# Kernel tuning notes

Hardware: AMD Instinct MI355X
Metric: run time of the kernel (lower is better)

## Reference

```python
import jax, jax.numpy as jnp
import numpy as np

N = 50000      # nodes
E = 800000     # edges (avg degree 16)
D = 128        # node_dim
H = 128        # hidden_dim
ED = 16        # edge_dim (unused by GCNConv, kept for signature fidelity)
G = 64         # graphs in batch
EPS = 1e-5     # BatchNorm eps


def setup_inputs() -> dict:
    key = jax.random.key(0)
    ks = jax.random.split(key, 16)
    s = 0.05
    inp = {
        "x": jax.random.normal(ks[0], (N, D), jnp.float32),
        "edge_index": jax.random.randint(ks[1], (2, E), 0, N, dtype=jnp.int64),
        "edge_attr": jax.random.normal(ks[2], (E, ED), jnp.float32),
        "batch": jnp.sort(jax.random.randint(ks[3], (N,), 0, G, dtype=jnp.int64)),
        # GCNConv weights/biases
        "W1": jax.random.normal(ks[4], (D, H), jnp.float32) * s,
        "b1": jnp.zeros((H,), jnp.float32),
        "W2": jax.random.normal(ks[5], (H, H), jnp.float32) * s,
        "b2": jnp.zeros((H,), jnp.float32),
        "W3": jax.random.normal(ks[6], (H, H), jnp.float32) * s,
        "b3": jnp.zeros((H,), jnp.float32),
        # BatchNorm affine params (training-mode batch stats)
        "g1": jnp.ones((H,), jnp.float32), "be1": jnp.zeros((H,), jnp.float32),
        "g2": jnp.ones((H,), jnp.float32), "be2": jnp.zeros((H,), jnp.float32),
        "g3": jnp.ones((H,), jnp.float32), "be3": jnp.zeros((H,), jnp.float32),
    }
    return inp


def reference(x, edge_index, edge_attr, batch,
              W1, b1, W2, b2, W3, b3,
              g1, be1, g2, be2, g3, be3):
    n = x.shape[0]
    src, dst = edge_index[0], edge_index[1]

    # GCN symmetric normalization with added self-loops:
    # deg[i] = 1 + in_degree(i); norm(e) = deg[src]^-1/2 * deg[dst]^-1/2
    deg = jax.ops.segment_sum(jnp.ones((src.shape[0],), x.dtype), dst,
                              num_segments=n) + 1.0
    dinv = jax.lax.rsqrt(deg)
    edge_norm = (dinv[src] * dinv[dst])[:, None]   # [E,1]
    self_norm = (dinv * dinv)[:, None]             # [N,1] self-loop weight

    def gcn(h, W, b):
        h = h @ W                                  # [N,H]
        agg = jax.ops.segment_sum(h[src] * edge_norm, dst, num_segments=n)
        return agg + h * self_norm + b

    def bn_sigmoid(h, g, b):
        m = h.mean(0)
        v = jnp.mean(jnp.square(h - m), 0)         # biased variance (torch BN)
        return jax.nn.sigmoid((h - m) * jax.lax.rsqrt(v + EPS) * g + b)

    h = bn_sigmoid(gcn(x, W1, b1), g1, be1)
    h = bn_sigmoid(gcn(h, W2, b2), g2, be2)
    h = bn_sigmoid(gcn(h, W3, b3), g3, be3)

    # global_mean_pool over graph ids
    cnt = jax.ops.segment_sum(jnp.ones((n,), h.dtype), batch, num_segments=G)
    pooled = jax.ops.segment_sum(h, batch, num_segments=G)
    return pooled / jnp.maximum(cnt, 1.0)[:, None]
```

## Files before the change

kernel.cpp:

```cpp
#include <hip/hip_runtime.h>
#include <math.h>

#define NDIM 128

typedef __attribute__((ext_vector_type(8))) short short8;
typedef __attribute__((ext_vector_type(4))) float f32x4;

__device__ __forceinline__ float sigmoidf_(float x){ return 1.0f/(1.0f + __expf(-x)); }

__device__ __forceinline__ unsigned short f2bf(float f){
  unsigned u = __float_as_uint(f);
  unsigned r = (u + 0x7fffu + ((u >> 16) & 1u)) >> 16;
  return (unsigned short)r;
}

__global__ void deg_count_k(const int* __restrict__ dst, int* __restrict__ counts, int E){
  int e = blockIdx.x*blockDim.x + threadIdx.x;
  if(e < E) atomicAdd(&counts[dst[e]], 1);
}

__global__ void dinv_k(const int* __restrict__ counts, float* __restrict__ dinv, int N){
  int i = blockIdx.x*blockDim.x + threadIdx.x;
  if(i < N) dinv[i] = rsqrtf(1.0f + (float)counts[i]);
}

__global__ void scan1_k(const int* __restrict__ counts, int* __restrict__ scanned,
                        int* __restrict__ chunksums, int N){
  __shared__ int lds[256];
  int t = threadIdx.x; int idx = blockIdx.x*256 + t;
  int x = (idx < N) ? counts[idx] : 0;
  lds[t] = x; __syncthreads();
  for(int o=1;o<256;o<<=1){
    int v = (t>=o) ? lds[t-o] : 0;
    __syncthreads();
    lds[t] += v;
    __syncthreads();
  }
  if(idx < N) scanned[idx] = lds[t];
  if(t == 255) chunksums[blockIdx.x] = lds[255];
}

__global__ void scan2_k(int* __restrict__ chunksums, int nchunks){
  __shared__ int lds[256];
  int t = threadIdx.x;
  int x = (t < nchunks) ? chunksums[t] : 0;
  lds[t] = x; __syncthreads();
  for(int o=1;o<256;o<<=1){
    int v = (t>=o) ? lds[t-o] : 0;
    __syncthreads();
    lds[t] += v;
    __syncthreads();
  }
  if(t < nchunks) chunksums[t] = lds[t] - x;
}

__global__ void scan3_k(const int* __restrict__ scanned, const int* __restrict__ counts,
                        const int* __restrict__ chunksums, int* __restrict__ row_start, int N){
  int i = blockIdx.x*blockDim.x + threadIdx.x;
  if(i < N) row_start[i] = scanned[i] - counts[i] + chunksums[i>>8];
}

__global__ void fill_k(const int* __restrict__ src, const int* __restrict__ dst,
                       const float* __restrict__ dinv, const int* __restrict__ row_start,
                       int* __restrict__ cursor, int* __restrict__ csr_src,
                       float* __restrict__ csr_norm, int E){
  int e = blockIdx.x*blockDim.x + threadIdx.x;
  if(e >= E) return;
  int d = dst[e], s = src[e];
  int pos = row_start[d] + atomicAdd(&cursor[d], 1);
  csr_src[pos] = s;
  csr_norm[pos] = dinv[s]*dinv[d];
}

__global__ void bounds_k(const int* __restrict__ batch, int* __restrict__ bound, int N, int G){
  int g = threadIdx.x;
  if(g > G) return;
  int lo = 0, hi = N;
  while(lo < hi){ int mid = (lo+hi)>>1; if(batch[mid] < g) lo = mid+1; else hi = mid; }
  bound[g] = lo;
}

__global__ void wprep_k(const float* __restrict__ W0, const float* __restrict__ W1,
                        const float* __restrict__ W2, unsigned short* __restrict__ Wsw){
  int t = blockIdx.x*256 + threadIdx.x;
  if(t >= 3*16384) return;
  int l = t >> 14; int i = t & 16383;
  const float* W = (l==0) ? W0 : ((l==1) ? W1 : W2);
  int k = i >> 7, n = i & 127;
  Wsw[l*16384 + (((k>>3)*128 + n)<<3) + (k&7)] = f2bf(W[k*128+n]);
}

__global__ __launch_bounds__(256) void gemm_mfma_k(const float* __restrict__ A,
                                                   const unsigned short* __restrict__ Wsw,
                                                   unsigned short* __restrict__ Bh,
                                                   const float* __restrict__ scale,
                                                   const float* __restrict__ shift,
                                                   int N){
  __shared__ unsigned short Al[16384];
  __shared__ unsigned short Wl[16384];
  int t = threadIdx.x;
  int row0 = blockIdx.x * 128;
  bool bn = (scale != nullptr);

  #pragma unroll
  for(int i=0;i<8;i++){
    int u = t + i*256;
    *(uint4*)&Wl[u<<3] = *(const uint4*)&Wsw[u<<3];
  }
  int o = t & 15, rbase = t >> 4;
  #pragma unroll
  for(int it=0; it<8; it++){
    int r = rbase + it*16;
    int grow = row0 + r;
    float4 v0 = make_float4(0.f,0.f,0.f,0.f), v1 = v0;
    if(grow < N){
      v0 = *(const float4*)&A[grow*NDIM + o*8];
      v1 = *(const float4*)&A[grow*NDIM + o*8 + 4];
      if(bn){
        float4 sc0 = *(const float4*)&scale[o*8],   sh0 = *(const float4*)&shift[o*8];
        float4 sc1 = *(const float4*)&scale[o*8+4], sh1 = *(const float4*)&shift[o*8+4];
        v0.x = sigmoidf_(v0.x*sc0.x + sh0.x); v0.y = sigmoidf_(v0.y*sc0.y + sh0.y);
        v0.z = sigmoidf_(v0.z*sc0.z + sh0.z); v0.w = sigmoidf_(v0.w*sc0.w + sh0.w);
        v1.x = sigmoidf_(v1.x*sc1.x + sh1.x); v1.y = sigmoidf_(v1.y*sc1.y + sh1.y);
        v1.z = sigmoidf_(v1.z*sc1.z + sh1.z); v1.w = sigmoidf_(v1.w*sc1.w + sh1.w);
      }
    }
    uint4 pk;
    pk.x = (unsigned)f2bf(v0.x) | ((unsigned)f2bf(v0.y)<<16);
    pk.y = (unsigned)f2bf(v0.z) | ((unsigned)f2bf(v0.w)<<16);
    pk.z = (unsigned)f2bf(v1.x) | ((unsigned)f2bf(v1.y)<<16);
    pk.w = (unsigned)f2bf(v1.z) | ((unsigned)f2bf(v1.w)<<16);
    *(uint4*)&Al[(o*128 + r)<<3] = pk;
  }
  __syncthreads();

  int wv = t >> 6, lane = t & 63, quad = lane >> 4, l16 = lane & 15;
  int rw = (wv & 1) * 64, cw = (wv >> 1) * 64;
  f32x4 acc[4][4];
  #pragma unroll
  for(int rt=0;rt<4;rt++)
    #pragma unroll
    for(int ct=0;ct<4;ct++) acc[rt][ct] = (f32x4){0.f,0.f,0.f,0.f};

  #pragma unroll
  for(int ks=0; ks<4; ks++){
    short8 a[4], b[4];
    #pragma unroll
    for(int rt=0;rt<4;rt++)
      a[rt] = *(short8*)&Al[(((ks*4+quad)*128) + rw + rt*16 + l16) << 3];
    #pragma unroll
    for(int ct=0;ct<4;ct++)
      b[ct] = *(short8*)&Wl[(((ks*4+quad)*128) + cw + ct*16 + l16) << 3];
    #pragma unroll
    for(int rt=0;rt<4;rt++)
      #pragma unroll
      for(int ct=0;ct<4;ct++)
        acc[rt][ct] = __builtin_amdgcn_mfma_f32_16x16x32_bf16(a[rt], b[ct], acc[rt][ct], 0, 0, 0);
  }

  #pragma unroll
  for(int rt=0;rt<4;rt++){
    int gr = row0 + rw + rt*16 + quad*4;
    #pragma unroll
    for(int ct=0;ct<4;ct++){
      int col = cw + ct*16 + l16;
      #pragma unroll
      for(int reg=0;reg<4;reg++){
        if(gr + reg < N) Bh[(gr+reg)*NDIM + col] = f2bf(acc[rt][ct][reg]);
      }
    }
  }
}

__global__ void agg_k(const unsigned int* __restrict__ hb,
                      const float* __restrict__ dinv,
                      const int* __restrict__ row_start, const int* __restrict__ counts,
                      const int* __restrict__ csr_src, const float* __restrict__ csr_norm,
                      const float* __restrict__ bias, float* __restrict__ hC, int N){
  int i = blockIdx.x;
  if(i >= N) return;
  int t = threadIdx.x;
  int rs = row_start[i], cnt = counts[i];
  float2 acc = make_float2(0.f, 0.f);
  int j = rs;
  for(; j+1 < rs+cnt; j += 2){
    int s0 = csr_src[j],   s1 = csr_src[j+1];
    float n0 = csr_norm[j], n1 = csr_norm[j+1];
    unsigned u0 = hb[s0*64 + t];
    unsigned u1 = hb[s1*64 + t];
    acc.x += n0*__uint_as_float(u0<<16) + n1*__uint_as_float(u1<<16);
    acc.y += n0*__uint_as_float(u0 & 0xffff0000u) + n1*__uint_as_float(u1 & 0xffff0000u);
  }
  if(j < rs+cnt){
    int s = csr_src[j]; float nm = csr_norm[j];
    unsigned u = hb[s*64 + t];
    acc.x += nm*__uint_as_float(u<<16);
    acc.y += nm*__uint_as_float(u & 0xffff0000u);
  }
  float di = dinv[i]; float sn = di*di;
  unsigned su = hb[i*64 + t];
  float2 bv = *(const float2*)&bias[t*2];
  float2 o;
  o.x = acc.x + sn*__uint_as_float(su<<16)           + bv.x;
  o.y = acc.y + sn*__uint_as_float(su & 0xffff0000u) + bv.y;
  *(float2*)&hC[i*NDIM + t*2] = o;
}

__global__ void stats_k(const float* __restrict__ h, float* __restrict__ sums,
                        float* __restrict__ sumsq, int N){
  __shared__ float ls[256], lq[256];
  int t = threadIdx.x;
  int f = t & 127, half = t >> 7;
  int rowsPerBlock = (N + gridDim.x - 1)/gridDim.x;
  int r0 = blockIdx.x * rowsPerBlock;
  int r1 = min(N, r0 + rowsPerBlock);
  float s=0.f, q=0.f;
  for(int r=r0+half; r<r1; r+=2){
    float v = h[r*NDIM + f];
    s += v; q += v*v;
  }
  ls[t]=s; lq[t]=q; __syncthreads();
  if(t < 128){
    s = ls[t] + ls[t+128];
    q = lq[t] + lq[t+128];
    atomicAdd(&sums[f], s);
    atomicAdd(&sumsq[f], q);
  }
}

__global__ void finalize_k(const float* __restrict__ sums, const float* __restrict__ sumsq,
                           const float* __restrict__ g, const float* __restrict__ be,
                           float* __restrict__ scale, float* __restrict__ shift, int N){
  int f = threadIdx.x;
  float invN = 1.0f/(float)N;
  float m = sums[f]*invN;
  float var = fmaxf(sumsq[f]*invN - m*m, 0.f);
  float s = g[f]*rsqrtf(var + 1e-5f);
  scale[f] = s;
  shift[f] = be[f] - m*s;
}

#define PCH 128
__global__ __launch_bounds__(256) void pool_k(const float* __restrict__ hC,
                                              const int* __restrict__ batch,
                                              const float* __restrict__ scale,
                                              const float* __restrict__ shift,
                                              float* __restrict__ out, int N){
  int t = threadIdx.x;
  int f = t & 127, half = t >> 7;
  int r0 = blockIdx.x*PCH + half;
  int r1 = min(N, blockIdx.x*PCH + PCH);
  float sc = scale[f], sh = shift[f];
  float acc = 0.f; int cur = -1;
  for(int r = r0; r < r1; r += 2){
    int g = batch[r];
    if(g != cur){
      if(cur >= 0) atomicAdd(&out[cur*NDIM + f], acc);
      acc = 0.f; cur = g;
    }
    acc += sigmoidf_(hC[r*NDIM + f]*sc + sh);
  }
  if(cur >= 0) atomicAdd(&out[cur*NDIM + f], acc);
}

__global__ void div_k(float* __restrict__ out, const int* __restrict__ bound){
  int g = blockIdx.x, f = threadIdx.x;
  float cnt = (float)(bound[g+1] - bound[g]);
  out[g*NDIM + f] /= fmaxf(cnt, 1.0f);
}

extern "C" void kernel_launch(void* const* d_in, const int* in_sizes, int n_in,
                              void* d_out, int out_size, void* d_ws, size_t ws_size,
                              hipStream_t stream){
  const float* x     = (const float*)d_in[0];
  const int*   ei    = (const int*)d_in[1];
  const int*   batch = (const int*)d_in[3];
  const float* W [3] = {(const float*)d_in[4], (const float*)d_in[6], (const float*)d_in[8]};
  const float* bi[3] = {(const float*)d_in[5], (const float*)d_in[7], (const float*)d_in[9]};
  const float* gg[3] = {(const float*)d_in[10], (const float*)d_in[12], (const float*)d_in[14]};
  const float* bb[3] = {(const float*)d_in[11], (const float*)d_in[13], (const float*)d_in[15]};

  int N = in_sizes[0] / NDIM;
  int E = in_sizes[1] / 2;
  int G = out_size / NDIM;
  const int* src = ei;
  const int* dst = ei + E;

  char* p = (char*)d_ws;
  auto alloc = [&](size_t bytes)->void*{
    void* r = (void*)p; p += (bytes + 255) & ~(size_t)255; return r;
  };
  unsigned short* hB  = (unsigned short*)alloc((size_t)N*NDIM*2);
  unsigned short* Wsw = (unsigned short*)alloc(3*16384*2);
  float* hC        = (float*)alloc((size_t)N*NDIM*4);
  int*   counts    = (int*)  alloc((size_t)N*4);
  int*   cursor    = (int*)  alloc((size_t)N*4);
  int*   scanned   = (int*)  alloc((size_t)N*4);
  int*   chunksums = (int*)  alloc(256*4);
  int*   row_start = (int*)  alloc((size_t)N*4);
  float* dinv      = (float*)alloc((size_t)N*4);
  int*   csr_src   = (int*)  alloc((size_t)E*4);
  float* csr_norm  = (float*)alloc((size_t)E*4);
  float* sums      = (float*)alloc(3*128*4);
  float* sumsq     = (float*)alloc(3*128*4);
  float* scale     = (float*)alloc(3*128*4);
  float* shift     = (float*)alloc(3*128*4);
  int*   bound     = (int*)  alloc(256*4);

  hipMemsetAsync(counts, 0, (size_t)N*4, stream);
  hipMemsetAsync(cursor, 0, (size_t)N*4, stream);
  hipMemsetAsync(sums,  0, 3*128*4, stream);
  hipMemsetAsync(sumsq, 0, 3*128*4, stream);
  hipMemsetAsync(d_out, 0, (size_t)out_size*4, stream);

  deg_count_k<<<(E+255)/256, 256, 0, stream>>>(dst, counts, E);
  dinv_k<<<(N+255)/256, 256, 0, stream>>>(counts, dinv, N);

  int nchunks = (N+255)/256;
  scan1_k<<<nchunks, 256, 0, stream>>>(counts, scanned, chunksums, N);
  scan2_k<<<1, 256, 0, stream>>>(chunksums, nchunks);
  scan3_k<<<(N+255)/256, 256, 0, stream>>>(scanned, counts, chunksums, row_start, N);
  fill_k<<<(E+255)/256, 256, 0, stream>>>(src, dst, dinv, row_start, cursor, csr_src, csr_norm, E);
  bounds_k<<<1, 128, 0, stream>>>(batch, bound, N, G);
  wprep_k<<<(3*16384+255)/256, 256, 0, stream>>>(W[0], W[1], W[2], Wsw);

  const float* hin = x;
  for(int l=0; l<3; l++){
    const float* sc = (l == 0) ? nullptr : (scale + (l-1)*128);
    const float* sh = (l == 0) ? nullptr : (shift + (l-1)*128);
    gemm_mfma_k<<<(N+127)/128, 256, 0, stream>>>(hin, Wsw + l*16384, hB, sc, sh, N);
    agg_k<<<N, 64, 0, stream>>>((const unsigned int*)hB, dinv, row_start, counts,
                                csr_src, csr_norm, bi[l], hC, N);
    stats_k<<<400, 256, 0, stream>>>(hC, sums + l*128, sumsq + l*128, N);
    finalize_k<<<1, 128, 0, stream>>>(sums + l*128, sumsq + l*128, gg[l], bb[l],
                                      scale + l*128, shift + l*128, N);
    hin = hC;
  }

  pool_k<<<(N+PCH-1)/PCH, 256, 0, stream>>>(hC, batch, scale + 2*128, shift + 2*128,
                                            (float*)d_out, N);
  div_k<<<G, 128, 0, stream>>>((float*)d_out, bound);
}
```

Before: 499.3 us.

## Pack CSR src/norm into uint2 and split wave across two edges per step

The CSR source index and edge norm are stored interleaved as one 8-byte record, so each edge needs one load instead of two separate arrays. The aggregation kernel now has each half-wave handle a different edge, each lane reading 8 bytes (4 bf16 features) per gather, with the loop unrolled 4 deep. The two halves are combined with a cross-lane shuffle at the end. This is meant to raise memory-level parallelism and cut the count of gather instructions, in exchange for a shuffle reduction and half the lanes sitting idle during the final write.

```diff
diff --git a/kernel.cpp b/kernel.cpp
--- a/kernel.cpp
+++ b/kernel.cpp
@@ -62,14 +62,15 @@
 
 __global__ void fill_k(const int* __restrict__ src, const int* __restrict__ dst,
                        const float* __restrict__ dinv, const int* __restrict__ row_start,
-                       int* __restrict__ cursor, int* __restrict__ csr_src,
-                       float* __restrict__ csr_norm, int E){
+                       int* __restrict__ cursor, uint2* __restrict__ csr, int E){
   int e = blockIdx.x*blockDim.x + threadIdx.x;
   if(e >= E) return;
   int d = dst[e], s = src[e];
   int pos = row_start[d] + atomicAdd(&cursor[d], 1);
-  csr_src[pos] = s;
-  csr_norm[pos] = dinv[s]*dinv[d];
+  uint2 rec;
+  rec.x = (unsigned)s;
+  rec.y = __float_as_uint(dinv[s]*dinv[d]);
+  csr[pos] = rec;
 }
 
 __global__ void bounds_k(const int* __restrict__ batch, int* __restrict__ bound, int N, int G){
@@ -172,38 +173,48 @@
   }
 }
 
-__global__ void agg_k(const unsigned int* __restrict__ hb,
+__global__ void agg_k(const uint2* __restrict__ hb2,
                       const float* __restrict__ dinv,
                       const int* __restrict__ row_start, const int* __restrict__ counts,
-                      const int* __restrict__ csr_src, const float* __restrict__ csr_norm,
+                      const uint2* __restrict__ csr,
                       const float* __restrict__ bias, float* __restrict__ hC, int N){
   int i = blockIdx.x;
   if(i >= N) return;
-  int t = threadIdx.x;
+  int lane = threadIdx.x;
+  int h = lane & 31, half = lane >> 5;
   int rs = row_start[i], cnt = counts[i];
-  float2 acc = make_float2(0.f, 0.f);
-  int j = rs;
-  for(; j+1 < rs+cnt; j += 2){
-    int s0 = csr_src[j],   s1 = csr_src[j+1];
-    float n0 = csr_norm[j], n1 = csr_norm[j+1];
-    unsigned u0 = hb[s0*64 + t];
-    unsigned u1 = hb[s1*64 + t];
-    acc.x += n0*__uint_as_float(u0<<16) + n1*__uint_as_float(u1<<16);
-    acc.y += n0*__uint_as_float(u0 & 0xffff0000u) + n1*__uint_as_float(u1 & 0xffff0000u);
-  }
-  if(j < rs+cnt){
-    int s = csr_src[j]; float nm = csr_norm[j];
-    unsigned u = hb[s*64 + t];
-    acc.x += nm*__uint_as_float(u<<16);
-    acc.y += nm*__uint_as_float(u & 0xffff0000u);
-  }
-  float di = dinv[i]; float sn = di*di;
-  unsigned su = hb[i*64 + t];
-  float2 bv = *(const float2*)&bias[t*2];
-  float2 o;
-  o.x = acc.x + sn*__uint_as_float(su<<16)           + bv.x;
-  o.y = acc.y + sn*__uint_as_float(su & 0xffff0000u) + bv.y;
-  *(float2*)&hC[i*NDIM + t*2] = o;
+  int re = rs + cnt;
+  float a0=0.f, a1=0.f, a2=0.f, a3=0.f;
+  for(int j0 = rs; j0 < re; j0 += 8){
+    #pragma unroll
+    for(int q=0; q<4; q++){
+      int j = j0 + 2*q + half;
+      if(j < re){
+        uint2 rec = csr[j];
+        float nm = __uint_as_float(rec.y);
+        uint2 u = hb2[(size_t)rec.x*32 + h];
+        a0 += nm*__uint_as_float(u.x<<16);
+        a1 += nm*__uint_as_float(u.x & 0xffff0000u);
+        a2 += nm*__uint_as_float(u.y<<16);
+        a3 += nm*__uint_as_float(u.y & 0xffff0000u);
+      }
+    }
+  }
+  a0 += __shfl(a0, h + 32);
+  a1 += __shfl(a1, h + 32);
+  a2 += __shfl(a2, h + 32);
+  a3 += __shfl(a3, h + 32);
+  if(half == 0){
+    float di = dinv[i], sn = di*di;
+    uint2 su = hb2[(size_t)i*32 + h];
+    float4 bv = *(const float4*)&bias[h*4];
+    float4 o;
+    o.x = a0 + sn*__uint_as_float(su.x<<16)           + bv.x;
+    o.y = a1 + sn*__uint_as_float(su.x & 0xffff0000u) + bv.y;
+    o.z = a2 + sn*__uint_as_float(su.y<<16)           + bv.z;
+    o.w = a3 + sn*__uint_as_float(su.y & 0xffff0000u) + bv.w;
+    *(float4*)&hC[i*NDIM + h*4] = o;
+  }
 }
 
 __global__ void stats_k(const float* __restrict__ h, float* __restrict__ sums,
@@ -299,8 +310,7 @@
   int*   chunksums = (int*)  alloc(256*4);
   int*   row_start = (int*)  alloc((size_t)N*4);
   float* dinv      = (float*)alloc((size_t)N*4);
-  int*   csr_src   = (int*)  alloc((size_t)E*4);
-  float* csr_norm  = (float*)alloc((size_t)E*4);
+  uint2* csr       = (uint2*)alloc((size_t)E*8);
   float* sums      = (float*)alloc(3*128*4);
   float* sumsq     = (float*)alloc(3*128*4);
   float* scale     = (float*)alloc(3*128*4);
@@ -320,7 +330,7 @@
   scan1_k<<<nchunks, 256, 0, stream>>>(counts, scanned, chunksums, N);
   scan2_k<<<1, 256, 0, stream>>>(chunksums, nchunks);
   scan3_k<<<(N+255)/256, 256, 0, stream>>>(scanned, counts, chunksums, row_start, N);
-  fill_k<<<(E+255)/256, 256, 0, stream>>>(src, dst, dinv, row_start, cursor, csr_src, csr_norm, E);
+  fill_k<<<(E+255)/256, 256, 0, stream>>>(src, dst, dinv, row_start, cursor, csr, E);
   bounds_k<<<1, 128, 0, stream>>>(batch, bound, N, G);
   wprep_k<<<(3*16384+255)/256, 256, 0, stream>>>(W[0], W[1], W[2], Wsw);
 
@@ -329,8 +339,8 @@
     const float* sc = (l == 0) ? nullptr : (scale + (l-1)*128);
     const float* sh = (l == 0) ? nullptr : (shift + (l-1)*128);
     gemm_mfma_k<<<(N+127)/128, 256, 0, stream>>>(hin, Wsw + l*16384, hB, sc, sh, N);
-    agg_k<<<N, 64, 0, stream>>>((const unsigned int*)hB, dinv, row_start, counts,
-                                csr_src, csr_norm, bi[l], hC, N);
+    agg_k<<<N, 64, 0, stream>>>((const uint2*)hB, dinv, row_start, counts,
+                                csr, bi[l], hC, N);
     stats_k<<<400, 256, 0, stream>>>(hC, sums + l*128, sumsq + l*128, N);
     finalize_k<<<1, 128, 0, stream>>>(sums + l*128, sumsq + l*128, gg[l], bb[l],
                                       scale + l*128, shift + l*128, N);
```

Result: slower. 538.5 us (+7.9%).

## Fuse BatchNorm stats into aggregation, pack CSR records, 4 rows per block

Applied to the files above, without the earlier changes.

Packs CSR source index and edge norm into one 8-byte record so each edge needs a single load. The aggregation kernel now processes four nodes per 256-thread block with a 4-way unrolled edge loop. It also accumulates per-feature sum and sum-of-squares in LDS and flushes them with global atomics, which removes the separate stats kernel and its full re-read of hC. The cost is LDS atomic contention and more global atomics (one flush per block, about 12.5k blocks) compared with the old 400-block stats pass.

```diff
diff --git a/kernel.cpp b/kernel.cpp
--- a/kernel.cpp
+++ b/kernel.cpp
@@ -62,14 +62,15 @@
 
 __global__ void fill_k(const int* __restrict__ src, const int* __restrict__ dst,
                        const float* __restrict__ dinv, const int* __restrict__ row_start,
-                       int* __restrict__ cursor, int* __restrict__ csr_src,
-                       float* __restrict__ csr_norm, int E){
+                       int* __restrict__ cursor, uint2* __restrict__ csr, int E){
   int e = blockIdx.x*blockDim.x + threadIdx.x;
   if(e >= E) return;
   int d = dst[e], s = src[e];
   int pos = row_start[d] + atomicAdd(&cursor[d], 1);
-  csr_src[pos] = s;
-  csr_norm[pos] = dinv[s]*dinv[d];
+  uint2 rec;
+  rec.x = (unsigned)s;
+  rec.y = __float_as_uint(dinv[s]*dinv[d]);
+  csr[pos] = rec;
 }
 
 __global__ void bounds_k(const int* __restrict__ batch, int* __restrict__ bound, int N, int G){
@@ -172,59 +173,59 @@
   }
 }
 
-__global__ void agg_k(const unsigned int* __restrict__ hb,
+__global__ __launch_bounds__(256) void agg_k(const unsigned int* __restrict__ hb,
                       const float* __restrict__ dinv,
                       const int* __restrict__ row_start, const int* __restrict__ counts,
-                      const int* __restrict__ csr_src, const float* __restrict__ csr_norm,
-                      const float* __restrict__ bias, float* __restrict__ hC, int N){
-  int i = blockIdx.x;
-  if(i >= N) return;
+                      const uint2* __restrict__ csr,
+                      const float* __restrict__ bias, float* __restrict__ hC,
+                      float* __restrict__ sums, float* __restrict__ sumsq, int N){
+  __shared__ float ls[NDIM], lq[NDIM];
   int t = threadIdx.x;
-  int rs = row_start[i], cnt = counts[i];
-  float2 acc = make_float2(0.f, 0.f);
-  int j = rs;
-  for(; j+1 < rs+cnt; j += 2){
-    int s0 = csr_src[j],   s1 = csr_src[j+1];
-    float n0 = csr_norm[j], n1 = csr_norm[j+1];
-    unsigned u0 = hb[s0*64 + t];
-    unsigned u1 = hb[s1*64 + t];
-    acc.x += n0*__uint_as_float(u0<<16) + n1*__uint_as_float(u1<<16);
-    acc.y += n0*__uint_as_float(u0 & 0xffff0000u) + n1*__uint_as_float(u1 & 0xffff0000u);
-  }
-  if(j < rs+cnt){
-    int s = csr_src[j]; float nm = csr_norm[j];
-    unsigned u = hb[s*64 + t];
-    acc.x += nm*__uint_as_float(u<<16);
-    acc.y += nm*__uint_as_float(u & 0xffff0000u);
-  }
-  float di = dinv[i]; float sn = di*di;
-  unsigned su = hb[i*64 + t];
-  float2 bv = *(const float2*)&bias[t*2];
-  float2 o;
-  o.x = acc.x + sn*__uint_as_float(su<<16)           + bv.x;
-  o.y = acc.y + sn*__uint_as_float(su & 0xffff0000u) + bv.y;
-  *(float2*)&hC[i*NDIM + t*2] = o;
-}
-
-__global__ void stats_k(const float* __restrict__ h, float* __restrict__ sums,
-                        float* __restrict__ sumsq, int N){
-  __shared__ float ls[256], lq[256];
-  int t = threadIdx.x;
-  int f = t & 127, half = t >> 7;
-  int rowsPerBlock = (N + gridDim.x - 1)/gridDim.x;
-  int r0 = blockIdx.x * rowsPerBlock;
-  int r1 = min(N, r0 + rowsPerBlock);
-  float s=0.f, q=0.f;
-  for(int r=r0+half; r<r1; r+=2){
-    float v = h[r*NDIM + f];
-    s += v; q += v*v;
-  }
-  ls[t]=s; lq[t]=q; __syncthreads();
-  if(t < 128){
-    s = ls[t] + ls[t+128];
-    q = lq[t] + lq[t+128];
-    atomicAdd(&sums[f], s);
-    atomicAdd(&sumsq[f], q);
+  if(t < NDIM){ ls[t] = 0.f; lq[t] = 0.f; }
+  __syncthreads();
+
+  int w = t >> 6, lane = t & 63;
+  int i = blockIdx.x*4 + w;
+  if(i < N){
+    int rs = row_start[i], re = rs + counts[i];
+    float2 acc = make_float2(0.f, 0.f);
+    int j = rs;
+    for(; j+3 < re; j += 4){
+      uint2 r0 = csr[j], r1 = csr[j+1], r2 = csr[j+2], r3 = csr[j+3];
+      unsigned u0 = hb[(size_t)r0.x*64 + lane];
+      unsigned u1 = hb[(size_t)r1.x*64 + lane];
+      unsigned u2 = hb[(size_t)r2.x*64 + lane];
+      unsigned u3 = hb[(size_t)r3.x*64 + lane];
+      float n0 = __uint_as_float(r0.y), n1 = __uint_as_float(r1.y);
+      float n2 = __uint_as_float(r2.y), n3 = __uint_as_float(r3.y);
+      acc.x += n0*__uint_as_float(u0<<16) + n1*__uint_as_float(u1<<16)
+             + n2*__uint_as_float(u2<<16) + n3*__uint_as_float(u3<<16);
+      acc.y += n0*__uint_as_float(u0 & 0xffff0000u) + n1*__uint_as_float(u1 & 0xffff0000u)
+             + n2*__uint_as_float(u2 & 0xffff0000u) + n3*__uint_as_float(u3 & 0xffff0000u);
+    }
+    for(; j < re; j++){
+      uint2 r0 = csr[j];
+      unsigned u0 = hb[(size_t)r0.x*64 + lane];
+      float n0 = __uint_as_float(r0.y);
+      acc.x += n0*__uint_as_float(u0<<16);
+      acc.y += n0*__uint_as_float(u0 & 0xffff0000u);
+    }
+    float di = dinv[i], sn = di*di;
+    unsigned su = hb[(size_t)i*64 + lane];
+    float2 bv = *(const float2*)&bias[lane*2];
+    float2 o;
+    o.x = acc.x + sn*__uint_as_float(su<<16)           + bv.x;
+    o.y = acc.y + sn*__uint_as_float(su & 0xffff0000u) + bv.y;
+    *(float2*)&hC[(size_t)i*NDIM + lane*2] = o;
+    atomicAdd(&ls[lane*2],   o.x);
+    atomicAdd(&ls[lane*2+1], o.y);
+    atomicAdd(&lq[lane*2],   o.x*o.x);
+    atomicAdd(&lq[lane*2+1], o.y*o.y);
+  }
+  __syncthreads();
+  if(t < NDIM){
+    atomicAdd(&sums[t],  ls[t]);
+    atomicAdd(&sumsq[t], lq[t]);
   }
 }
 
@@ -299,8 +300,7 @@
   int*   chunksums = (int*)  alloc(256*4);
   int*   row_start = (int*)  alloc((size_t)N*4);
   float* dinv      = (float*)alloc((size_t)N*4);
-  int*   csr_src   = (int*)  alloc((size_t)E*4);
-  float* csr_norm  = (float*)alloc((size_t)E*4);
+  uint2* csr       = (uint2*)alloc((size_t)E*8);
   float* sums      = (float*)alloc(3*128*4);
   float* sumsq     = (float*)alloc(3*128*4);
   float* scale     = (float*)alloc(3*128*4);
@@ -320,7 +320,7 @@
   scan1_k<<<nchunks, 256, 0, stream>>>(counts, scanned, chunksums, N);
   scan2_k<<<1, 256, 0, stream>>>(chunksums, nchunks);
   scan3_k<<<(N+255)/256, 256, 0, stream>>>(scanned, counts, chunksums, row_start, N);
-  fill_k<<<(E+255)/256, 256, 0, stream>>>(src, dst, dinv, row_start, cursor, csr_src, csr_norm, E);
+  fill_k<<<(E+255)/256, 256, 0, stream>>>(src, dst, dinv, row_start, cursor, csr, E);
   bounds_k<<<1, 128, 0, stream>>>(batch, bound, N, G);
   wprep_k<<<(3*16384+255)/256, 256, 0, stream>>>(W[0], W[1], W[2], Wsw);
 
@@ -329,9 +329,8 @@
     const float* sc = (l == 0) ? nullptr : (scale + (l-1)*128);
     const float* sh = (l == 0) ? nullptr : (shift + (l-1)*128);
     gemm_mfma_k<<<(N+127)/128, 256, 0, stream>>>(hin, Wsw + l*16384, hB, sc, sh, N);
-    agg_k<<<N, 64, 0, stream>>>((const unsigned int*)hB, dinv, row_start, counts,
-                                csr_src, csr_norm, bi[l], hC, N);
-    stats_k<<<400, 256, 0, stream>>>(hC, sums + l*128, sumsq + l*128, N);
+    agg_k<<<(N+3)/4, 256, 0, stream>>>((const unsigned int*)hB, dinv, row_start, counts,
+                                       csr, bi[l], hC, sums + l*128, sumsq + l*128, N);
     finalize_k<<<1, 128, 0, stream>>>(sums + l*128, sumsq + l*128, gg[l], bb[l],
                                       scale + l*128, shift + l*128, N);
     hin = hC;
```

After: 1.282 ms. 157% more time.
